# Performance work log

Hardware: AMD Instinct MI355X
Metric: run time of the kernel (lower is better)

## Reference

```python
import jax, jax.numpy as jnp
import numpy as np

EMBED_DIM = 1024
ATTN_DIM = 1024
BATCH = 4
SEQ = 2048


def setup_inputs() -> dict:
    key = jax.random.key(0)
    k1, k2, k3, k4 = jax.random.split(key, 4)
    embedded = jax.random.normal(k1, (BATCH, SEQ, EMBED_DIM), dtype=jnp.float32)
    # torch Linear weights have shape [out_features, in_features]
    scale = 1.0 / np.sqrt(EMBED_DIM)
    W_K = jax.random.uniform(k2, (ATTN_DIM, EMBED_DIM), dtype=jnp.float32, minval=-scale, maxval=scale)
    W_Q = jax.random.uniform(k3, (ATTN_DIM, EMBED_DIM), dtype=jnp.float32, minval=-scale, maxval=scale)
    W_V = jax.random.uniform(k4, (ATTN_DIM, EMBED_DIM), dtype=jnp.float32, minval=-scale, maxval=scale)
    return {"embedded": embedded, "W_K": W_K, "W_Q": W_Q, "W_V": W_V}


def reference(embedded, W_K, W_Q, W_V):
    # embedded: [B, L, E]; W_*: [A, E] (torch Linear layout, applied as x @ W.T)
    L = embedded.shape[1]
    A = W_K.shape[0]
    K = jnp.einsum('ble,ae->bla', embedded, W_K)
    Q = jnp.einsum('ble,ae->bla', embedded, W_Q)
    V = jnp.einsum('ble,ae->bla', embedded, W_V)
    att = jnp.einsum('bqa,bka->bqk', Q, K) / jnp.sqrt(jnp.float32(A))  # [B, L, L]
    causal = jnp.tril(jnp.ones((L, L), dtype=bool))  # lower-triangular mask
    att = jnp.where(causal, att, -jnp.inf)
    att = jax.nn.softmax(att, axis=-1)
    return jnp.einsum('bqk,bka->bqa', att, V)
```

## Files before the change

### kernel.cpp

```cpp
#include <hip/hip_runtime.h>
#include <hip/hip_bf16.h>
#include <stdint.h>

#define BATCH 4
#define SEQ   2048
#define EMB   1024
#define ADIM  1024

typedef __attribute__((ext_vector_type(8))) short  short8;
typedef __attribute__((ext_vector_type(4))) float  float4v;

static __device__ __forceinline__ unsigned short f2bf(float f) {
    unsigned int u = __float_as_uint(f);
    u += 0x7FFFu + ((u >> 16) & 1u);
    return (unsigned short)(u >> 16);
}

static __device__ __forceinline__ uint2 pack4(float4v v) {
    uint2 r;
    r.x = (unsigned)f2bf(v.x) | ((unsigned)f2bf(v.y) << 16);
    r.y = (unsigned)f2bf(v.z) | ((unsigned)f2bf(v.w) << 16);
    return r;
}

static __device__ __forceinline__ void gload16(const void* g, void* l) {
    __builtin_amdgcn_global_load_lds(
        (const __attribute__((address_space(1))) void*)g,
        (__attribute__((address_space(3))) void*)l, 16, 0, 0);
}

static __device__ __forceinline__ int swz8(int row) { return ((row >> 1) & 3) << 3; }

__global__ __launch_bounds__(256) void prep_kernel(
    const float* __restrict__ X,  const float* __restrict__ Wv,
    const float* __restrict__ Wq, const float* __restrict__ Wk,
    unsigned short* __restrict__ Xb, unsigned short* __restrict__ Wvb,
    unsigned short* __restrict__ WqT, unsigned short* __restrict__ WkT,
    float* __restrict__ rowsum)
{
    __shared__ unsigned short T[64][72];
    const int bI = blockIdx.x;
    if (bI < 4608) {
        const float* src; unsigned short* dst; int off;
        if (bI < 4096) { src = X;  dst = Xb;  off = bI; }
        else           { src = Wv; dst = Wvb; off = bI - 4096; }
        const int i = (off * 256 + threadIdx.x) * 8;
        float4v a = *(const float4v*)(src + i);
        float4v b = *(const float4v*)(src + i + 4);
        uint2 pa = pack4(a), pb = pack4(b);
        uint4 o; o.x = pa.x; o.y = pa.y; o.z = pb.x; o.w = pb.y;
        *(uint4*)(dst + i) = o;
        return;
    }
    if (bI < 4616) {
        const int i = ((bI - 4608) * 256 + threadIdx.x) * 4;
        *(float4v*)(rowsum + i) = float4v{0.f, 0.f, 0.f, 0.f};
        return;
    }
    const int z    = (bI - 4616) >> 8;
    const int tile = (bI - 4616) & 255;
    const int ti = tile >> 4;
    const int tj = tile & 15;
    const float* W = z ? Wk : Wq;
    unsigned short* WT = z ? WkT : WqT;
    const int t  = threadIdx.x;
    const int r  = t >> 2;
    const int c  = (t & 3) << 4;

    const float* src = W + (size_t)(ti * 64 + r) * EMB + tj * 64 + c;
    #pragma unroll
    for (int u = 0; u < 4; ++u) {
        float4v v = *(const float4v*)(src + 4 * u);
        uint2 p = pack4(v);
        *(uint2*)&T[r][c + 4 * u] = p;
    }
    __syncthreads();
    unsigned short tmp[16];
    #pragma unroll
    for (int u = 0; u < 16; ++u) tmp[u] = T[c + u][r];
    unsigned short* dst = WT + (size_t)(tj * 64 + r) * EMB + ti * 64 + c;
    *(uint4*)(dst)     = *(uint4*)&tmp[0];
    *(uint4*)(dst + 8) = *(uint4*)&tmp[8];
}

static __device__ __forceinline__ void gemm_core(
    const unsigned short* __restrict__ A, const unsigned short* __restrict__ B,
    int lda, int ldb, int m0, int n0, int klen,
    unsigned short* As, unsigned short* Bs, float4v acc[4][4])
{
    const int tid  = threadIdx.x;
    const int r    = tid >> 2;
    const int c8   = ((tid & 3) << 3) ^ swz8(tid >> 2);
    const int lane = tid & 63;
    const int wave = tid >> 6;
    const int quad = lane >> 4;
    const int l16  = lane & 15;
    const int wm   = (wave >> 1) << 6;
    const int wn   = (wave & 1) << 6;

    const unsigned short* Ag = A + (size_t)(m0 + r) * lda + c8;
    const unsigned short* Bg = B + (size_t)(n0 + r) * ldb + c8;
    unsigned short* Al = As + tid * 8;
    unsigned short* Bl = Bs + tid * 8;
    const int niter = klen >> 5;

    #define ISSUE(k0, st) do { \
        unsigned short* al_ = Al + (st) * 4096; \
        unsigned short* bl_ = Bl + (st) * 4096; \
        gload16(Ag + (k0),                    al_); \
        gload16(Ag + (k0) + (size_t)64 * lda, al_ + 2048); \
        gload16(Bg + (k0),                    bl_); \
        gload16(Bg + (k0) + (size_t)64 * ldb, bl_ + 2048); \
    } while (0)

    ISSUE(0, 0);
    ISSUE(32, 1);

    int ci = 0, ii = 2;
    for (int it = 0; it < niter; ++it) {
        const int knext = (it + 2 < niter) ? ((it + 2) << 5) : 0;
        ISSUE(knext, ii);
        asm volatile("s_waitcnt vmcnt(8)" ::: "memory");
        asm volatile("s_barrier" ::: "memory");

        const unsigned short* Ah = As + ci * 4096;
        const unsigned short* Bh = Bs + ci * 4096;
        short8 af[4], bfr[4];
        #pragma unroll
        for (int i = 0; i < 4; ++i) {
            const int row = wm + 16 * i + l16;
            af[i] = *(const short8*)&Ah[row * 32 + ((quad * 8) ^ swz8(row))];
        }
        #pragma unroll
        for (int j = 0; j < 4; ++j) {
            const int row = wn + 16 * j + l16;
            bfr[j] = *(const short8*)&Bh[row * 32 + ((quad * 8) ^ swz8(row))];
        }
        #pragma unroll
        for (int i = 0; i < 4; ++i)
            #pragma unroll
            for (int j = 0; j < 4; ++j)
                acc[i][j] = __builtin_amdgcn_mfma_f32_16x16x32_bf16(af[i], bfr[j], acc[i][j], 0, 0, 0);

        asm volatile("s_barrier" ::: "memory");
        ci = (ci == 2) ? 0 : ci + 1;
        ii = (ii == 2) ? 0 : ii + 1;
    }
    asm volatile("s_waitcnt vmcnt(0)" ::: "memory");
    #undef ISSUE
}

#define DECL_TILE_IDX() \
    const int lane = threadIdx.x & 63; \
    const int wave = threadIdx.x >> 6; \
    const int quad = lane >> 4; \
    const int l16  = lane & 15; \
    const int wm   = (wave >> 1) << 6; \
    const int wn   = (wave & 1) << 6;

__global__ __launch_bounds__(256, 3) void m_kernel(
    const unsigned short* __restrict__ WkT, const unsigned short* __restrict__ WqT,
    float* __restrict__ Mtf)
{
    __shared__ __align__(16) unsigned short As[3 * 128 * 32];
    __shared__ __align__(16) unsigned short Bs[3 * 128 * 32];
    const int idx = blockIdx.x;
    const int kc  = idx >> 6;
    const int t   = idx & 63;
    const int m0  = (t >> 3) << 7;
    const int n0  = (t & 7) << 7;

    float4v acc[4][4];
    #pragma unroll
    for (int i = 0; i < 4; ++i)
        #pragma unroll
        for (int j = 0; j < 4; ++j)
            acc[i][j] = float4v{0.f, 0.f, 0.f, 0.f};

    gemm_core(WkT + kc * 256, WqT + kc * 256, EMB, EMB, m0, n0, 256, As, Bs, acc);

    float* dst = Mtf + (size_t)kc * 1024 * 1024;
    DECL_TILE_IDX();
    #pragma unroll
    for (int i = 0; i < 4; ++i)
        #pragma unroll
        for (int j = 0; j < 4; ++j)
            #pragma unroll
            for (int rr = 0; rr < 4; ++rr) {
                const int row = m0 + wm + 16 * i + quad * 4 + rr;
                const int col = n0 + wn + 16 * j + l16;
                dst[(size_t)row * EMB + col] = acc[i][j][rr];
            }
}

__global__ __launch_bounds__(256) void mc_kernel(
    const float* __restrict__ Mtf, unsigned short* __restrict__ Mt)
{
    const int base = (blockIdx.x * 256 + threadIdx.x) * 16;
    #pragma unroll
    for (int u = 0; u < 4; ++u) {
        const int i = base + u * 4;
        float4v s = *(const float4v*)(Mtf + i);
        s = s + *(const float4v*)(Mtf + 1048576 + i);
        s = s + *(const float4v*)(Mtf + 2097152 + i);
        s = s + *(const float4v*)(Mtf + 3145728 + i);
        s = s * 0.03125f;
        uint2 p = pack4(s);
        *(uint2*)(Mt + i) = p;
    }
}

__global__ __launch_bounds__(512, 2) void qv_kernel(
    const unsigned short* __restrict__ Xb, const unsigned short* __restrict__ Mt,
    const unsigned short* __restrict__ Wvb,
    unsigned short* __restrict__ Qpb, unsigned short* __restrict__ Vtb)
{
    __shared__ __align__(16) unsigned short LDS[49152];
    unsigned short* As = LDS;
    unsigned short* Bs = LDS + 24576;

    const int idx  = blockIdx.x;
    const int mt   = ((idx & 7) << 2) | ((idx >> 3) & 3);
    const int slot = idx >> 5;
    const int z    = slot >> 2;
    const int n0   = (slot & 3) << 8;
    const int m0   = mt << 8;
    const unsigned short* B = z ? Wvb : Mt;

    const int tid  = threadIdx.x;
    const int lane = tid & 63;
    const int wave = tid >> 6;
    const int quad = lane >> 4;
    const int l16  = lane & 15;
    const int wm   = (wave >> 2) << 7;
    const int wn   = (wave & 3) << 6;

    const int srow = tid >> 2;
    const int c8   = ((tid & 3) << 3) ^ swz8(srow);

    const unsigned short* Ag0 = Xb + (size_t)(m0 + srow) * EMB + c8;
    const unsigned short* Ag1 = Ag0 + (size_t)128 * EMB;
    const unsigned short* Bg0 = B  + (size_t)(n0 + srow) * EMB + c8;
    const unsigned short* Bg1 = Bg0 + (size_t)128 * EMB;
    unsigned short* Al = As + tid * 8;
    unsigned short* Bl = Bs + tid * 8;

    #define ISSUE_QA(t, st) do { \
        gload16(Ag0 + (t) * 32, Al + (st) * 8192); \
        gload16(Ag1 + (t) * 32, Al + (st) * 8192 + 4096); \
    } while (0)
    #define ISSUE_QB(t, st) do { \
        gload16(Bg0 + (t) * 32, Bl + (st) * 8192); \
        gload16(Bg1 + (t) * 32, Bl + (st) * 8192 + 4096); \
    } while (0)

    float4v acc[8][4];
    #pragma unroll
    for (int i = 0; i < 8; ++i)
        #pragma unroll
        for (int j = 0; j < 4; ++j)
            acc[i][j] = float4v{0.f, 0.f, 0.f, 0.f};

    ISSUE_QA(0, 0); ISSUE_QB(0, 0);
    ISSUE_QA(1, 1); ISSUE_QB(1, 1);

    int ci = 0, ii = 2;
    for (int it = 0; it < 32; ++it) {
        const int tn = (it + 2 < 32) ? (it + 2) : 0;
        const unsigned short* Ah = As + ci * 8192;
        const unsigned short* Bh = Bs + ci * 8192;

        ISSUE_QA(tn, ii);
        asm volatile("s_waitcnt vmcnt(6)" ::: "memory");
        asm volatile("s_barrier" ::: "memory");

        short8 af[8], bfr[4];
        #pragma unroll
        for (int i = 0; i < 4; ++i) {
            const int row = wm + 16 * i + l16;
            af[i] = *(const short8*)&Ah[row * 32 + ((quad * 8) ^ swz8(row))];
        }
        #pragma unroll
        for (int j = 0; j < 4; ++j) {
            const int row = wn + 16 * j + l16;
            bfr[j] = *(const short8*)&Bh[row * 32 + ((quad * 8) ^ swz8(row))];
        }
        #pragma unroll
        for (int i = 0; i < 4; ++i) {
            const int row = wm + 64 + 16 * i + l16;
            af[4 + i] = *(const short8*)&Ah[row * 32 + ((quad * 8) ^ swz8(row))];
        }

        __builtin_amdgcn_s_setprio(1);
        #pragma unroll
        for (int i = 0; i < 4; ++i)
            #pragma unroll
            for (int j = 0; j < 4; ++j)
                acc[i][j] = __builtin_amdgcn_mfma_f32_16x16x32_bf16(af[i], bfr[j], acc[i][j], 0, 0, 0);
        __builtin_amdgcn_s_setprio(0);

        ISSUE_QB(tn, ii);

        __builtin_amdgcn_s_setprio(1);
        #pragma unroll
        for (int i = 0; i < 4; ++i)
            #pragma unroll
            for (int j = 0; j < 4; ++j)
                acc[i + 4][j] = __builtin_amdgcn_mfma_f32_16x16x32_bf16(af[4 + i], bfr[j], acc[i + 4][j], 0, 0, 0);
        __builtin_amdgcn_s_setprio(0);

        asm volatile("s_barrier" ::: "memory");
        ci = (ci == 2) ? 0 : ci + 1;
        ii = (ii == 2) ? 0 : ii + 1;
    }
    asm volatile("s_waitcnt vmcnt(0)" ::: "memory");
    #undef ISSUE_QA
    #undef ISSUE_QB

    if (z == 0) {
        #pragma unroll
        for (int i = 0; i < 8; ++i)
            #pragma unroll
            for (int j = 0; j < 4; ++j)
                #pragma unroll
                for (int rr = 0; rr < 4; ++rr) {
                    const int row = m0 + wm + ((i & 3) << 4) + ((i >> 2) << 6) + quad * 4 + rr;
                    const int col = n0 + wn + 16 * j + l16;
                    Qpb[(size_t)row * ADIM + col] = f2bf(acc[i][j][rr]);
                }
    } else {
        const int bb = m0 >> 11;
        const int l0 = m0 & (SEQ - 1);
        #pragma unroll
        for (int h = 0; h < 2; ++h) {
            __syncthreads();
            if ((wm >> 7) == h) {
                #pragma unroll
                for (int i = 0; i < 8; ++i)
                    #pragma unroll
                    for (int j = 0; j < 4; ++j) {
                        const int qloc = ((i & 3) << 4) + ((i >> 2) << 6) + quad * 4;
                        const int acol = wn + 16 * j + l16;
                        uint2 w;
                        w.x = (unsigned)f2bf(acc[i][j][0]) | ((unsigned)f2bf(acc[i][j][1]) << 16);
                        w.y = (unsigned)f2bf(acc[i][j][2]) | ((unsigned)f2bf(acc[i][j][3]) << 16);
                        *(uint2*)&LDS[acol * 136 + qloc] = w;
                    }
            }
            __syncthreads();
            const int acol = tid >> 1;
            const int qh   = (tid & 1) << 6;
            unsigned short* dst = Vtb + (((size_t)(bb * ADIM + n0 + acol)) << 11)
                                      + l0 + h * 128 + qh;
            #pragma unroll
            for (int u = 0; u < 8; ++u)
                *(uint4*)(dst + u * 8) = *(const uint4*)&LDS[acol * 136 + qh + u * 8];
        }
    }
}

__global__ __launch_bounds__(256, 3) void s_kernel(
    const unsigned short* __restrict__ Qpb, const unsigned short* __restrict__ Xb,
    unsigned short* __restrict__ E, float* __restrict__ rowsum)
{
    const int idx = blockIdx.x;
    const int b   = idx & 3;
    const int tri = idx >> 2;
    int qt = 0;
    while (((qt + 1) * (qt + 2)) / 2 <= tri) ++qt;
    const int kt = tri - (qt * (qt + 1)) / 2;
    const int q0 = qt << 7;
    const int k0 = kt << 7;

    __shared__ __align__(16) unsigned short As[3 * 128 * 32];
    __shared__ __align__(16) unsigned short Bs[3 * 128 * 32];

    float4v acc[4][4];
    #pragma unroll
    for (int i = 0; i < 4; ++i)
        #pragma unroll
        for (int j = 0; j < 4; ++j)
            acc[i][j] = float4v{0.f, 0.f, 0.f, 0.f};

    gemm_core(Qpb + (size_t)b * SEQ * ADIM, Xb + (size_t)b * SEQ * EMB,
              ADIM, EMB, q0, k0, EMB, As, Bs, acc);

    unsigned short* Eb = E + (size_t)b * SEQ * SEQ;
    float* rsb = rowsum + (size_t)b * SEQ;
    DECL_TILE_IDX();
    #pragma unroll
    for (int i = 0; i < 4; ++i)
        #pragma unroll
        for (int rr = 0; rr < 4; ++rr) {
            const int row = q0 + wm + 16 * i + quad * 4 + rr;
            float s = 0.f;
            #pragma unroll
            for (int j = 0; j < 4; ++j) {
                const int col = k0 + wn + 16 * j + l16;
                float e = (col <= row) ? __expf(acc[i][j][rr]) : 0.f;
                s += e;
                Eb[(size_t)row * SEQ + col] = f2bf(e);
            }
            s += __shfl_xor(s, 1);
            s += __shfl_xor(s, 2);
            s += __shfl_xor(s, 4);
            s += __shfl_xor(s, 8);
            if (l16 == 0) atomicAdd(&rsb[row], s);
        }
}

__global__ __launch_bounds__(256, 3) void pv_kernel(
    const unsigned short* __restrict__ E, const unsigned short* __restrict__ Vtb,
    const float* __restrict__ rowsum, float* __restrict__ out)
{
    const int idx = blockIdx.x;
    const int t   = (idx < 256) ? (15 - (idx >> 5)) : ((idx - 256) >> 5);
    const int rem = idx & 31;
    const int b   = rem >> 3;
    const int a0  = (rem & 7) << 7;
    const int q0  = t << 7;

    __shared__ __align__(16) unsigned short As[3 * 128 * 32];
    __shared__ __align__(16) unsigned short Bs[3 * 128 * 32];

    float4v acc[4][4];
    #pragma unroll
    for (int i = 0; i < 4; ++i)
        #pragma unroll
        for (int j = 0; j < 4; ++j)
            acc[i][j] = float4v{0.f, 0.f, 0.f, 0.f};

    gemm_core(E + (size_t)b * SEQ * SEQ, Vtb + (size_t)b * ADIM * SEQ,
              SEQ, SEQ, q0, a0, q0 + 128, As, Bs, acc);

    float* ob = out + (size_t)b * SEQ * ADIM;
    const float* rsb = rowsum + (size_t)b * SEQ;
    DECL_TILE_IDX();
    #pragma unroll
    for (int i = 0; i < 4; ++i)
        #pragma unroll
        for (int rr = 0; rr < 4; ++rr) {
            const int row = q0 + wm + 16 * i + quad * 4 + rr;
            const float inv = 1.0f / rsb[row];
            #pragma unroll
            for (int j = 0; j < 4; ++j) {
                const int col = a0 + wn + 16 * j + l16;
                ob[(size_t)row * ADIM + col] = acc[i][j][rr] * inv;
            }
        }
}

extern "C" void kernel_launch(void* const* d_in, const int* in_sizes, int n_in,
                              void* d_out, int out_size, void* d_ws, size_t ws_size,
                              hipStream_t stream)
{
    const float* X  = (const float*)d_in[0];
    const float* Wk = (const float*)d_in[1];
    const float* Wq = (const float*)d_in[2];
    const float* Wv = (const float*)d_in[3];
    float* out = (float*)d_out;

    const size_t MB = 1024 * 1024;
    char* ws = (char*)d_ws;
    unsigned short* Xb  = (unsigned short*)(ws);
    unsigned short* Wvb = (unsigned short*)(ws + 16 * MB);
    unsigned short* WqT = (unsigned short*)(ws + 18 * MB);
    unsigned short* WkT = (unsigned short*)(ws + 20 * MB);
    unsigned short* Mt  = (unsigned short*)(ws + 22 * MB);
    unsigned short* Qpb = (unsigned short*)(ws + 24 * MB);
    unsigned short* E   = (unsigned short*)(ws + 40 * MB);
    unsigned short* Vtb = (unsigned short*)(ws + 72 * MB);
    float*          rowsum = (float*)(ws + 88 * MB);
    float*          Mtf = (float*)(ws + 40 * MB);

    hipLaunchKernelGGL(prep_kernel, dim3(5128), dim3(256), 0, stream,
                       X, Wv, Wq, Wk, Xb, Wvb, WqT, WkT, rowsum);
    hipLaunchKernelGGL(m_kernel, dim3(256), dim3(256), 0, stream, WkT, WqT, Mtf);
    hipLaunchKernelGGL(mc_kernel, dim3(256), dim3(256), 0, stream, Mtf, Mt);
    hipLaunchKernelGGL(qv_kernel, dim3(256), dim3(512), 0, stream,
                       Xb, Mt, Wvb, Qpb, Vtb);
    hipLaunchKernelGGL(s_kernel, dim3(4 * 136), dim3(256), 0, stream, Qpb, Xb, E, rowsum);
    hipLaunchKernelGGL(pv_kernel, dim3(512), dim3(256), 0, stream, E, Vtb, rowsum, out);
}
```

Before: 224.1 us.

## Use BK=64 double-buffered K pipeline with 8-chunk XOR swizzle in qv_kernel

Restructures the qv GEMM main loop from a triple-buffered BK=32 pipeline (32 iterations) to a double-buffered BK=64 pipeline (16 iterations), doubling LDS use to 128 KB and dropping occupancy to one block per CU. Global loads move to a 64-column-per-row layout with an XOR swizzle over 8 chunks, and each iteration runs two 32-wide k-substeps. The aim is to halve barrier and loop overhead per unit of work. The cost is less latency hiding, since there is one prefetch stage instead of two and fewer resident blocks.

```diff
diff --git a/kernel.cpp b/kernel.cpp
--- a/kernel.cpp
+++ b/kernel.cpp
@@ -210,14 +210,14 @@
     }
 }
 
-__global__ __launch_bounds__(512, 2) void qv_kernel(
+__global__ __launch_bounds__(512, 1) void qv_kernel(
     const unsigned short* __restrict__ Xb, const unsigned short* __restrict__ Mt,
     const unsigned short* __restrict__ Wvb,
     unsigned short* __restrict__ Qpb, unsigned short* __restrict__ Vtb)
 {
-    __shared__ __align__(16) unsigned short LDS[49152];
+    __shared__ __align__(16) unsigned short LDS[65536];
     unsigned short* As = LDS;
-    unsigned short* Bs = LDS + 24576;
+    unsigned short* Bs = LDS + 32768;
 
     const int idx  = blockIdx.x;
     const int mt   = ((idx & 7) << 2) | ((idx >> 3) & 3);
@@ -235,23 +235,24 @@
     const int wm   = (wave >> 2) << 7;
     const int wn   = (wave & 3) << 6;
 
-    const int srow = tid >> 2;
-    const int c8   = ((tid & 3) << 3) ^ swz8(srow);
-
-    const unsigned short* Ag0 = Xb + (size_t)(m0 + srow) * EMB + c8;
-    const unsigned short* Ag1 = Ag0 + (size_t)128 * EMB;
-    const unsigned short* Bg0 = B  + (size_t)(n0 + srow) * EMB + c8;
-    const unsigned short* Bg1 = Bg0 + (size_t)128 * EMB;
+    const int r8 = tid >> 3;
+    const int sg = (tid & 7) ^ (r8 & 7);
+
+    const unsigned short* Ag = Xb + (size_t)(m0 + r8) * EMB + sg * 8;
+    const unsigned short* Bg = B  + (size_t)(n0 + r8) * EMB + sg * 8;
     unsigned short* Al = As + tid * 8;
     unsigned short* Bl = Bs + tid * 8;
 
-    #define ISSUE_QA(t, st) do { \
-        gload16(Ag0 + (t) * 32, Al + (st) * 8192); \
-        gload16(Ag1 + (t) * 32, Al + (st) * 8192 + 4096); \
-    } while (0)
-    #define ISSUE_QB(t, st) do { \
-        gload16(Bg0 + (t) * 32, Bl + (st) * 8192); \
-        gload16(Bg1 + (t) * 32, Bl + (st) * 8192 + 4096); \
+    #define ISSUE_T(t64, st) do { \
+        const size_t ko_ = (size_t)(t64) * 64; \
+        gload16(Ag + ko_,                       Al + (st) * 16384); \
+        gload16(Ag + ko_ + (size_t)64  * EMB,   Al + (st) * 16384 + 4096); \
+        gload16(Ag + ko_ + (size_t)128 * EMB,   Al + (st) * 16384 + 8192); \
+        gload16(Ag + ko_ + (size_t)192 * EMB,   Al + (st) * 16384 + 12288); \
+        gload16(Bg + ko_,                       Bl + (st) * 16384); \
+        gload16(Bg + ko_ + (size_t)64  * EMB,   Bl + (st) * 16384 + 4096); \
+        gload16(Bg + ko_ + (size_t)128 * EMB,   Bl + (st) * 16384 + 8192); \
+        gload16(Bg + ko_ + (size_t)192 * EMB,   Bl + (st) * 16384 + 12288); \
     } while (0)
 
     float4v acc[8][4];
@@ -261,61 +262,62 @@
         for (int j = 0; j < 4; ++j)
             acc[i][j] = float4v{0.f, 0.f, 0.f, 0.f};
 
-    ISSUE_QA(0, 0); ISSUE_QB(0, 0);
-    ISSUE_QA(1, 1); ISSUE_QB(1, 1);
-
-    int ci = 0, ii = 2;
-    for (int it = 0; it < 32; ++it) {
-        const int tn = (it + 2 < 32) ? (it + 2) : 0;
-        const unsigned short* Ah = As + ci * 8192;
-        const unsigned short* Bh = Bs + ci * 8192;
-
-        ISSUE_QA(tn, ii);
-        asm volatile("s_waitcnt vmcnt(6)" ::: "memory");
+    ISSUE_T(0, 0);
+
+    for (int it = 0; it < 16; ++it) {
+        const int tn = (it + 1 < 16) ? (it + 1) : 0;
+        ISSUE_T(tn, (it + 1) & 1);
+        asm volatile("s_waitcnt vmcnt(8)" ::: "memory");
         asm volatile("s_barrier" ::: "memory");
 
-        short8 af[8], bfr[4];
-        #pragma unroll
-        for (int i = 0; i < 4; ++i) {
-            const int row = wm + 16 * i + l16;
-            af[i] = *(const short8*)&Ah[row * 32 + ((quad * 8) ^ swz8(row))];
-        }
-        #pragma unroll
-        for (int j = 0; j < 4; ++j) {
-            const int row = wn + 16 * j + l16;
-            bfr[j] = *(const short8*)&Bh[row * 32 + ((quad * 8) ^ swz8(row))];
-        }
-        #pragma unroll
-        for (int i = 0; i < 4; ++i) {
-            const int row = wm + 64 + 16 * i + l16;
-            af[4 + i] = *(const short8*)&Ah[row * 32 + ((quad * 8) ^ swz8(row))];
-        }
-
-        __builtin_amdgcn_s_setprio(1);
-        #pragma unroll
-        for (int i = 0; i < 4; ++i)
-            #pragma unroll
-            for (int j = 0; j < 4; ++j)
-                acc[i][j] = __builtin_amdgcn_mfma_f32_16x16x32_bf16(af[i], bfr[j], acc[i][j], 0, 0, 0);
-        __builtin_amdgcn_s_setprio(0);
-
-        ISSUE_QB(tn, ii);
-
-        __builtin_amdgcn_s_setprio(1);
-        #pragma unroll
-        for (int i = 0; i < 4; ++i)
-            #pragma unroll
-            for (int j = 0; j < 4; ++j)
-                acc[i + 4][j] = __builtin_amdgcn_mfma_f32_16x16x32_bf16(af[4 + i], bfr[j], acc[i + 4][j], 0, 0, 0);
-        __builtin_amdgcn_s_setprio(0);
+        const unsigned short* Ah = As + (it & 1) * 16384;
+        const unsigned short* Bh = Bs + (it & 1) * 16384;
+
+        {
+            short8 af[8], bfr[4];
+            #pragma unroll
+            for (int i = 0; i < 8; ++i) {
+                const int row = wm + 16 * i + l16;
+                af[i] = *(const short8*)&Ah[row * 64 + ((quad ^ (row & 7)) << 3)];
+            }
+            #pragma unroll
+            for (int j = 0; j < 4; ++j) {
+                const int row = wn + 16 * j + l16;
+                bfr[j] = *(const short8*)&Bh[row * 64 + ((quad ^ (row & 7)) << 3)];
+            }
+            __builtin_amdgcn_s_setprio(1);
+            #pragma unroll
+            for (int i = 0; i < 8; ++i)
+                #pragma unroll
+                for (int j = 0; j < 4; ++j)
+                    acc[i][j] = __builtin_amdgcn_mfma_f32_16x16x32_bf16(af[i], bfr[j], acc[i][j], 0, 0, 0);
+            __builtin_amdgcn_s_setprio(0);
+        }
+        {
+            short8 af[8], bfr[4];
+            #pragma unroll
+            for (int i = 0; i < 8; ++i) {
+                const int row = wm + 16 * i + l16;
+                af[i] = *(const short8*)&Ah[row * 64 + (((4 + quad) ^ (row & 7)) << 3)];
+            }
+            #pragma unroll
+            for (int j = 0; j < 4; ++j) {
+                const int row = wn + 16 * j + l16;
+                bfr[j] = *(const short8*)&Bh[row * 64 + (((4 + quad) ^ (row & 7)) << 3)];
+            }
+            __builtin_amdgcn_s_setprio(1);
+            #pragma unroll
+            for (int i = 0; i < 8; ++i)
+                #pragma unroll
+                for (int j = 0; j < 4; ++j)
+                    acc[i][j] = __builtin_amdgcn_mfma_f32_16x16x32_bf16(af[i], bfr[j], acc[i][j], 0, 0, 0);
+            __builtin_amdgcn_s_setprio(0);
+        }
 
         asm volatile("s_barrier" ::: "memory");
-        ci = (ci == 2) ? 0 : ci + 1;
-        ii = (ii == 2) ? 0 : ii + 1;
     }
     asm volatile("s_waitcnt vmcnt(0)" ::: "memory");
-    #undef ISSUE_QA
-    #undef ISSUE_QB
+    #undef ISSUE_T
 
     if (z == 0) {
         #pragma unroll
@@ -324,7 +326,7 @@
             for (int j = 0; j < 4; ++j)
                 #pragma unroll
                 for (int rr = 0; rr < 4; ++rr) {
-                    const int row = m0 + wm + ((i & 3) << 4) + ((i >> 2) << 6) + quad * 4 + rr;
+                    const int row = m0 + wm + 16 * i + quad * 4 + rr;
                     const int col = n0 + wn + 16 * j + l16;
                     Qpb[(size_t)row * ADIM + col] = f2bf(acc[i][j][rr]);
                 }
@@ -339,7 +341,7 @@
                 for (int i = 0; i < 8; ++i)
                     #pragma unroll
                     for (int j = 0; j < 4; ++j) {
-                        const int qloc = ((i & 3) << 4) + ((i >> 2) << 6) + quad * 4;
+                        const int qloc = 16 * i + quad * 4;
                         const int acol = wn + 16 * j + l16;
                         uint2 w;
                         w.x = (unsigned)f2bf(acc[i][j][0]) | ((unsigned)f2bf(acc[i][j][1]) << 16);
```

New measurement: 223.5 us. Within noise of the previous version (-0.2%).
